# Performance work log

Hardware: AMD Instinct MI355X
Metric: run time of the kernel (lower is better)

Reference implementation:

```python
import jax, jax.numpy as jnp
import numpy as np

E, TOP_K, H, I = 8, 2, 1024, 2048
B, S = 1, 2048


def setup_inputs() -> dict:
    key = jax.random.key(0)
    ks = jax.random.split(key, 5)
    scale_h = 1.0 / np.sqrt(H)
    scale_i = 1.0 / np.sqrt(I)
    return {
        "hidden_states": jax.random.normal(ks[0], (B, S, H), dtype=jnp.float32),
        "gate_w": jax.random.normal(ks[1], (E, H), dtype=jnp.float32) * scale_h,
        "w1": jax.random.normal(ks[2], (E, I, H), dtype=jnp.float32) * scale_h,
        "w3": jax.random.normal(ks[3], (E, I, H), dtype=jnp.float32) * scale_h,
        "w2": jax.random.normal(ks[4], (E, H, I), dtype=jnp.float32) * scale_i,
    }


def _moe(x, gate_w, w1, w3, w2):
    orig_shape = x.shape
    xt = x.reshape(-1, H)                       # [T, H]
    logits = xt @ gate_w.T                      # [T, E] router logits
    probs = jax.nn.softmax(logits, axis=-1)
    topw, topi = jax.lax.top_k(probs, TOP_K)    # [T, K]
    topw = topw / jnp.sum(topw, axis=-1, keepdims=True)  # renormalize=True
    # dense per-token expert weights [T, E]
    ew = jnp.sum(jax.nn.one_hot(topi, E, dtype=xt.dtype) * topw[..., None], axis=1)
    # SwiGLU experts, vectorized over all experts
    g = jnp.einsum('th,eih->tei', xt, w1)       # [T, E, I]
    u = jnp.einsum('th,eih->tei', xt, w3)
    act = jax.nn.silu(g) * u
    ye = jnp.einsum('tei,ehi->teh', act, w2)    # [T, E, H]
    out = jnp.einsum('te,teh->th', ew, ye)      # weighted combine
    return out.reshape(orig_shape)


def reference(hidden_states, gate_w, w1, w3, w2):
    return _moe(hidden_states, gate_w, w1, w3, w2)
```

## Files before the change

kernel.cpp:

```cpp
#include <hip/hip_runtime.h>
#include <hip/hip_bf16.h>
#include <math.h>

#define T_TOK 2048
#define HD 1024
#define ID 2048
#define NE 8

typedef __attribute__((ext_vector_type(8))) short s16x8;
typedef __attribute__((ext_vector_type(8))) unsigned short u16x8;
typedef __attribute__((ext_vector_type(4))) float f32x4;
typedef __attribute__((ext_vector_type(4))) unsigned short u16x4;

__device__ __forceinline__ unsigned short f2bf(float f) {
  union { float f; unsigned u; } v; v.f = f;
  unsigned r = v.u + 0x7FFFu + ((v.u >> 16) & 1u);
  return (unsigned short)(r >> 16);
}

__device__ __forceinline__ s16x8 cvt8(float4 a, float4 b) {
  union { s16x8 v; __hip_bfloat16 h[8]; } u;
  u.h[0] = __float2bfloat16(a.x); u.h[1] = __float2bfloat16(a.y);
  u.h[2] = __float2bfloat16(a.z); u.h[3] = __float2bfloat16(a.w);
  u.h[4] = __float2bfloat16(b.x); u.h[5] = __float2bfloat16(b.y);
  u.h[6] = __float2bfloat16(b.z); u.h[7] = __float2bfloat16(b.w);
  return u.v;
}

#define GLOAD16(gsrc, ldst) \
  __builtin_amdgcn_global_load_lds((const __attribute__((address_space(1))) void*)(gsrc), \
                                   (__attribute__((address_space(3))) void*)(ldst), 16, 0, 0)

#define WAIT_BARRIER() do { \
  asm volatile("s_waitcnt vmcnt(0) lgkmcnt(0)" ::: "memory"); \
  __builtin_amdgcn_s_barrier(); } while (0)

__global__ void router_k(const float* __restrict__ x, const float* __restrict__ gate,
                         int* __restrict__ cnt, int* __restrict__ tok,
                         float* __restrict__ wt, int* __restrict__ inv) {
  int wid = threadIdx.x >> 6, lane = threadIdx.x & 63;
  int t = blockIdx.x * 4 + wid;
  const float* xr = x + (size_t)t * HD;
  float acc[NE];
#pragma unroll
  for (int e = 0; e < NE; e++) acc[e] = 0.f;
  for (int h = lane; h < HD; h += 64) {
    float xv = xr[h];
#pragma unroll
    for (int e = 0; e < NE; e++) acc[e] += xv * gate[e * HD + h];
  }
#pragma unroll
  for (int e = 0; e < NE; e++)
    for (int off = 32; off; off >>= 1) acc[e] += __shfl_xor(acc[e], off);
  int i0 = 0;
#pragma unroll
  for (int e = 1; e < NE; e++) if (acc[e] > acc[i0]) i0 = e;
  int i1 = (i0 == 0) ? 1 : 0;
#pragma unroll
  for (int e = 0; e < NE; e++) if (e != i0 && acc[e] > acc[i1]) i1 = e;
  float w0 = 1.f / (1.f + expf(acc[i1] - acc[i0]));
  float w1 = 1.f - w0;
  if (lane == 0) {
    int p0 = atomicAdd(&cnt[i0], 1);
    tok[i0 * T_TOK + p0] = t; wt[i0 * T_TOK + p0] = w0;
    inv[2 * t] = (i0 << 16) | p0;
    int p1 = atomicAdd(&cnt[i1], 1);
    tok[i1 * T_TOK + p1] = t; wt[i1 * T_TOK + p1] = w1;
    inv[2 * t + 1] = (i1 << 16) | p1;
  }
}

__global__ void prefix_k(const int* __restrict__ cnt, int* __restrict__ offs) {
  if (threadIdx.x == 0) {
    int s = 0;
    for (int e = 0; e < NE; e++) { offs[e] = s; s += cnt[e]; }
  }
}

__global__ void gather_k(const float* __restrict__ x, const int* __restrict__ cnt,
                         const int* __restrict__ offs, const int* __restrict__ tok,
                         unsigned short* __restrict__ Xg) {
  int e = blockIdx.x >> 11, slot = blockIdx.x & 2047;
  if (slot >= cnt[e]) return;
  int t = tok[e * T_TOK + slot];
  int row = offs[e] + slot;
  int c = threadIdx.x * 4;
  float4 f = *(const float4*)(x + (size_t)t * HD + c);
  u16x4 o; o.x = f2bf(f.x); o.y = f2bf(f.y); o.z = f2bf(f.z); o.w = f2bf(f.w);
  *(u16x4*)(Xg + (size_t)row * HD + c) = o;
}

__global__ __launch_bounds__(512, 4) void gemm1_k(
    const unsigned short* __restrict__ Xg, const float* __restrict__ w1,
    const float* __restrict__ w3, const int* __restrict__ cnt,
    const int* __restrict__ offs, const float* __restrict__ wt,
    unsigned short* __restrict__ act) {
  int bid = blockIdx.x;
  int e = bid & 7;
  int r2 = bid >> 3;
  int nt = r2 & 31, mt = r2 >> 5;
  int count = cnt[e];
  if (mt * 256 >= count) return;
  int i0 = nt * 64;
  int rbase = offs[e] + mt * 256;
  const float* W1 = w1 + (size_t)e * ID * HD;
  const float* W3 = w3 + (size_t)e * ID * HD;

  __shared__ __align__(16) unsigned short Ab[2][256 * 32];
  __shared__ __align__(16) float B1b[2][64 * 32];
  __shared__ __align__(16) float B2b[2][64 * 32];

  int tid = threadIdx.x;
  int wid = tid >> 6, lane = tid & 63;
  int wr = wid >> 1, wc = wid & 1;
  int l15 = lane & 15, hi = lane >> 4;

  const unsigned short* aS[2];
#pragma unroll
  for (int c = 0; c < 2; c++)
    aS[c] = Xg + (size_t)(rbase + c * 128 + wid * 16 + (lane >> 2)) * HD
               + (((lane & 3) ^ ((lane >> 2) & 3)) * 8);
  const float* b1S = W1 + (size_t)(i0 + wid * 8 + (lane >> 3)) * HD
                        + (((lane & 7) ^ ((lane >> 3) & 7)) * 4);
  const float* b2S = W3 + (size_t)(i0 + wid * 8 + (lane >> 3)) * HD
                        + (((lane & 7) ^ ((lane >> 3) & 7)) * 4);

  f32x4 accg[4][2], accu[4][2];
#pragma unroll
  for (int m = 0; m < 4; m++)
#pragma unroll
    for (int n = 0; n < 2; n++) {
      accg[m][n] = (f32x4){0.f, 0.f, 0.f, 0.f};
      accu[m][n] = (f32x4){0.f, 0.f, 0.f, 0.f};
    }

  int aswz = (hi ^ (l15 & 3)) * 8;
  int bg0 = ((hi * 2) ^ (l15 & 7)) * 4;
  int bg1 = ((hi * 2 + 1) ^ (l15 & 7)) * 4;

#define G1_STAGE(buf, k0) do { \
    GLOAD16(aS[0] + (k0), &Ab[buf][wid * 512]); \
    GLOAD16(aS[1] + (k0), &Ab[buf][4096 + wid * 512]); \
    GLOAD16(b1S + (k0), &B1b[buf][wid * 256]); \
    GLOAD16(b2S + (k0), &B2b[buf][wid * 256]); } while (0)

  G1_STAGE(0, 0);
  WAIT_BARRIER();

  for (int t = 0; t < 32; ++t) {
    int cur = t & 1;
    if (t < 31) G1_STAGE(cur ^ 1, (t + 1) * 32);
    s16x8 a[4];
#pragma unroll
    for (int m = 0; m < 4; m++)
      a[m] = *(const s16x8*)&Ab[cur][(wr * 64 + m * 16 + l15) * 32 + aswz];
#pragma unroll
    for (int n = 0; n < 2; n++) {
      int rB = (wc * 32 + n * 16 + l15) * 32;
      float4 q0 = *(const float4*)&B1b[cur][rB + bg0];
      float4 q1 = *(const float4*)&B1b[cur][rB + bg1];
      s16x8 b1 = cvt8(q0, q1);
      float4 q2 = *(const float4*)&B2b[cur][rB + bg0];
      float4 q3 = *(const float4*)&B2b[cur][rB + bg1];
      s16x8 b2 = cvt8(q2, q3);
#pragma unroll
      for (int m = 0; m < 4; m++) {
        accg[m][n] = __builtin_amdgcn_mfma_f32_16x16x32_bf16(a[m], b1, accg[m][n], 0, 0, 0);
        accu[m][n] = __builtin_amdgcn_mfma_f32_16x16x32_bf16(a[m], b2, accu[m][n], 0, 0, 0);
      }
    }
    WAIT_BARRIER();
  }

#pragma unroll
  for (int m = 0; m < 4; m++)
#pragma unroll
    for (int r = 0; r < 4; r++) {
      int rl = mt * 256 + wr * 64 + m * 16 + hi * 4 + r;
      if (rl < count) {
        float w = wt[e * T_TOK + rl];
#pragma unroll
        for (int n = 0; n < 2; n++) {
          float g = accg[m][n][r], u = accu[m][n][r];
          float s = (g / (1.f + expf(-g))) * u * w;
          act[(size_t)(offs[e] + rl) * ID + i0 + wc * 32 + n * 16 + l15] =
              (unsigned short)__bfloat16_as_ushort(__float2bfloat16(s));
        }
      }
    }
#undef G1_STAGE
}

__global__ __launch_bounds__(512, 4) void gemm2_k(
    const unsigned short* __restrict__ act, const float* __restrict__ w2,
    const int* __restrict__ cnt, const int* __restrict__ offs,
    float* __restrict__ ye) {
  int bid = blockIdx.x;
  int e = bid & 7;
  int r2 = bid >> 3;
  int nt = r2 & 15, mt = r2 >> 4;
  int count = cnt[e];
  if (mt * 256 >= count) return;
  int h0 = nt * 64;
  int rbase = offs[e] + mt * 256;
  const float* W2 = w2 + (size_t)e * HD * ID;

  __shared__ __align__(16) unsigned short Ab[2][256 * 32];
  __shared__ __align__(16) float Bb[2][64 * 32];

  int tid = threadIdx.x;
  int wid = tid >> 6, lane = tid & 63;
  int wr = wid >> 1, wc = wid & 1;
  int l15 = lane & 15, hi = lane >> 4;

  const unsigned short* aS[2];
#pragma unroll
  for (int c = 0; c < 2; c++)
    aS[c] = act + (size_t)(rbase + c * 128 + wid * 16 + (lane >> 2)) * ID
                + (((lane & 3) ^ ((lane >> 2) & 3)) * 8);
  const float* bS = W2 + (size_t)(h0 + wid * 8 + (lane >> 3)) * ID
                       + (((lane & 7) ^ ((lane >> 3) & 7)) * 4);

  f32x4 acc[4][2];
#pragma unroll
  for (int m = 0; m < 4; m++)
#pragma unroll
    for (int n = 0; n < 2; n++) acc[m][n] = (f32x4){0.f, 0.f, 0.f, 0.f};

  int aswz = (hi ^ (l15 & 3)) * 8;
  int bg0 = ((hi * 2) ^ (l15 & 7)) * 4;
  int bg1 = ((hi * 2 + 1) ^ (l15 & 7)) * 4;

#define G2_STAGE(buf, k0) do { \
    GLOAD16(aS[0] + (k0), &Ab[buf][wid * 512]); \
    GLOAD16(aS[1] + (k0), &Ab[buf][4096 + wid * 512]); \
    GLOAD16(bS + (k0), &Bb[buf][wid * 256]); } while (0)

  G2_STAGE(0, 0);
  WAIT_BARRIER();

  for (int t = 0; t < 64; ++t) {
    int cur = t & 1;
    if (t < 63) G2_STAGE(cur ^ 1, (t + 1) * 32);
    s16x8 a[4];
#pragma unroll
    for (int m = 0; m < 4; m++)
      a[m] = *(const s16x8*)&Ab[cur][(wr * 64 + m * 16 + l15) * 32 + aswz];
#pragma unroll
    for (int n = 0; n < 2; n++) {
      int rB = (wc * 32 + n * 16 + l15) * 32;
      float4 q0 = *(const float4*)&Bb[cur][rB + bg0];
      float4 q1 = *(const float4*)&Bb[cur][rB + bg1];
      s16x8 b = cvt8(q0, q1);
#pragma unroll
      for (int m = 0; m < 4; m++)
        acc[m][n] = __builtin_amdgcn_mfma_f32_16x16x32_bf16(a[m], b, acc[m][n], 0, 0, 0);
    }
    WAIT_BARRIER();
  }

#pragma unroll
  for (int m = 0; m < 4; m++)
#pragma unroll
    for (int r = 0; r < 4; r++) {
      int slot = mt * 256 + wr * 64 + m * 16 + hi * 4 + r;
      if (slot < count) {
#pragma unroll
        for (int n = 0; n < 2; n++)
          ye[(size_t)(offs[e] + slot) * HD + h0 + wc * 32 + n * 16 + l15] = acc[m][n][r];
      }
    }
#undef G2_STAGE
}

__global__ void combine_k(const float* __restrict__ ye, const int* __restrict__ inv,
                          const int* __restrict__ offs, float* __restrict__ out) {
  int t = blockIdx.x;
  int c = threadIdx.x * 4;
  int v0 = inv[2 * t], v1 = inv[2 * t + 1];
  int r0 = offs[v0 >> 16] + (v0 & 0xFFFF);
  int r1 = offs[v1 >> 16] + (v1 & 0xFFFF);
  float4 a = *(const float4*)(ye + (size_t)r0 * HD + c);
  float4 b = *(const float4*)(ye + (size_t)r1 * HD + c);
  float4 o = {a.x + b.x, a.y + b.y, a.z + b.z, a.w + b.w};
  *(float4*)(out + (size_t)t * HD + c) = o;
}

extern "C" void kernel_launch(void* const* d_in, const int* in_sizes, int n_in,
                              void* d_out, int out_size, void* d_ws, size_t ws_size,
                              hipStream_t stream) {
  const float* x    = (const float*)d_in[0];
  const float* gate = (const float*)d_in[1];
  const float* w1   = (const float*)d_in[2];
  const float* w3   = (const float*)d_in[3];
  const float* w2   = (const float*)d_in[4];
  float* out = (float*)d_out;

  char* ws = (char*)d_ws;
  int* cnt  = (int*)(ws + 0);
  int* offs = (int*)(ws + 256);
  int* tok  = (int*)(ws + 512);
  float* wt = (float*)(ws + 66048);
  int* inv  = (int*)(ws + 131584);
  unsigned short* Xg  = (unsigned short*)(ws + 148480);
  unsigned short* act = (unsigned short*)(ws + 10634240);
  float* ye = (float*)(ws + 31605760);

  hipMemsetAsync(cnt, 0, 256, stream);

  router_k<<<T_TOK / 4, 256, 0, stream>>>(x, gate, cnt, tok, wt, inv);
  prefix_k<<<1, 64, 0, stream>>>(cnt, offs);
  gather_k<<<NE * T_TOK, 256, 0, stream>>>(x, cnt, offs, tok, Xg);
  gemm1_k<<<NE * 32 * 4, 512, 0, stream>>>(Xg, w1, w3, cnt, offs, wt, act);
  gemm2_k<<<NE * 16 * 4, 512, 0, stream>>>(act, w2, cnt, offs, ye);
  combine_k<<<T_TOK, 256, 0, stream>>>(ye, inv, offs, out);
}
```

Baseline: 405.4 us.

## Deepen weight prefetch pipeline, relayout LDS tiles, and shrink gemm2 tiles

Both expert GEMMs move from a double-buffered load/compute loop with full vmcnt(0) waits to a deeper pipeline. gemm1 gets a triple-buffered weight stage and gemm2 a quad-buffered one, each waiting with a partial vmcnt and a single barrier per iteration. The LDS layout is changed from XOR-swizzled rows to a k-chunk-major layout that matches the MFMA fragment reads. gemm2 is cut to 256 threads with 128-row tiles and the gemm1 grid is enlarged, which aims to hide global-load latency and raise occupancy at the cost of more LDS, more redundant weight reads, and some fragile wait-count logic.

```diff
diff --git a/kernel.cpp b/kernel.cpp
--- a/kernel.cpp
+++ b/kernel.cpp
@@ -30,10 +30,6 @@
 #define GLOAD16(gsrc, ldst) \
   __builtin_amdgcn_global_load_lds((const __attribute__((address_space(1))) void*)(gsrc), \
                                    (__attribute__((address_space(3))) void*)(ldst), 16, 0, 0)
-
-#define WAIT_BARRIER() do { \
-  asm volatile("s_waitcnt vmcnt(0) lgkmcnt(0)" ::: "memory"); \
-  __builtin_amdgcn_s_barrier(); } while (0)
 
 __global__ void router_k(const float* __restrict__ x, const float* __restrict__ gate,
                          int* __restrict__ cnt, int* __restrict__ tok,
@@ -107,8 +103,8 @@
   const float* W3 = w3 + (size_t)e * ID * HD;
 
   __shared__ __align__(16) unsigned short Ab[2][256 * 32];
-  __shared__ __align__(16) float B1b[2][64 * 32];
-  __shared__ __align__(16) float B2b[2][64 * 32];
+  __shared__ __align__(16) float B1b[3][64 * 32];
+  __shared__ __align__(16) float B2b[3][64 * 32];
 
   int tid = threadIdx.x;
   int wid = tid >> 6, lane = tid & 63;
@@ -118,12 +114,13 @@
   const unsigned short* aS[2];
 #pragma unroll
   for (int c = 0; c < 2; c++)
-    aS[c] = Xg + (size_t)(rbase + c * 128 + wid * 16 + (lane >> 2)) * HD
-               + (((lane & 3) ^ ((lane >> 2) & 3)) * 8);
-  const float* b1S = W1 + (size_t)(i0 + wid * 8 + (lane >> 3)) * HD
-                        + (((lane & 7) ^ ((lane >> 3) & 7)) * 4);
-  const float* b2S = W3 + (size_t)(i0 + wid * 8 + (lane >> 3)) * HD
-                        + (((lane & 7) ^ ((lane >> 3) & 7)) * 4);
+    aS[c] = Xg + (size_t)(rbase + (2 * wid + c) * 16 + l15) * HD + hi * 8;
+  int aD[2];
+#pragma unroll
+  for (int c = 0; c < 2; c++) aD[c] = (2 * wid + c) * 512 + lane * 8;
+  const float* b1S = W1 + (size_t)(i0 + lane) * HD + wid * 4;
+  const float* b2S = W3 + (size_t)(i0 + lane) * HD + wid * 4;
+  int bD = wid * 256 + lane * 4;
 
   f32x4 accg[4][2], accu[4][2];
 #pragma unroll
@@ -134,34 +131,36 @@
       accu[m][n] = (f32x4){0.f, 0.f, 0.f, 0.f};
     }
 
-  int aswz = (hi ^ (l15 & 3)) * 8;
-  int bg0 = ((hi * 2) ^ (l15 & 7)) * 4;
-  int bg1 = ((hi * 2 + 1) ^ (l15 & 7)) * 4;
-
-#define G1_STAGE(buf, k0) do { \
-    GLOAD16(aS[0] + (k0), &Ab[buf][wid * 512]); \
-    GLOAD16(aS[1] + (k0), &Ab[buf][4096 + wid * 512]); \
-    GLOAD16(b1S + (k0), &B1b[buf][wid * 256]); \
-    GLOAD16(b2S + (k0), &B2b[buf][wid * 256]); } while (0)
-
-  G1_STAGE(0, 0);
-  WAIT_BARRIER();
+#define STAGE_A1(buf, k0) do { \
+    GLOAD16(aS[0] + (k0), &Ab[buf][aD[0]]); \
+    GLOAD16(aS[1] + (k0), &Ab[buf][aD[1]]); } while (0)
+#define STAGE_B1(buf, k0) do { \
+    GLOAD16(b1S + (k0), &B1b[buf][bD]); \
+    GLOAD16(b2S + (k0), &B2b[buf][bD]); } while (0)
+
+  STAGE_A1(0, 0);
+  STAGE_B1(0, 0);
+  STAGE_B1(1, 32);
 
   for (int t = 0; t < 32; ++t) {
-    int cur = t & 1;
-    if (t < 31) G1_STAGE(cur ^ 1, (t + 1) * 32);
+    if (t < 31) asm volatile("s_waitcnt vmcnt(2)" ::: "memory");
+    else        asm volatile("s_waitcnt vmcnt(0)" ::: "memory");
+    __builtin_amdgcn_s_barrier();
+    if (t < 31) STAGE_A1((t + 1) & 1, (t + 1) * 32);
+    if (t < 30) STAGE_B1((t + 2) % 3, (t + 2) * 32);
+    int ab = t & 1, bb = t % 3;
     s16x8 a[4];
 #pragma unroll
     for (int m = 0; m < 4; m++)
-      a[m] = *(const s16x8*)&Ab[cur][(wr * 64 + m * 16 + l15) * 32 + aswz];
+      a[m] = *(const s16x8*)&Ab[ab][(wr * 4 + m) * 512 + hi * 128 + l15 * 8];
 #pragma unroll
     for (int n = 0; n < 2; n++) {
-      int rB = (wc * 32 + n * 16 + l15) * 32;
-      float4 q0 = *(const float4*)&B1b[cur][rB + bg0];
-      float4 q1 = *(const float4*)&B1b[cur][rB + bg1];
+      int rB = (wc * 32 + n * 16 + l15) * 4;
+      float4 q0 = *(const float4*)&B1b[bb][(2 * hi) * 256 + rB];
+      float4 q1 = *(const float4*)&B1b[bb][(2 * hi + 1) * 256 + rB];
       s16x8 b1 = cvt8(q0, q1);
-      float4 q2 = *(const float4*)&B2b[cur][rB + bg0];
-      float4 q3 = *(const float4*)&B2b[cur][rB + bg1];
+      float4 q2 = *(const float4*)&B2b[bb][(2 * hi) * 256 + rB];
+      float4 q3 = *(const float4*)&B2b[bb][(2 * hi + 1) * 256 + rB];
       s16x8 b2 = cvt8(q2, q3);
 #pragma unroll
       for (int m = 0; m < 4; m++) {
@@ -169,7 +168,6 @@
         accu[m][n] = __builtin_amdgcn_mfma_f32_16x16x32_bf16(a[m], b2, accu[m][n], 0, 0, 0);
       }
     }
-    WAIT_BARRIER();
   }
 
 #pragma unroll
@@ -183,15 +181,15 @@
         for (int n = 0; n < 2; n++) {
           float g = accg[m][n][r], u = accu[m][n][r];
           float s = (g / (1.f + expf(-g))) * u * w;
-          act[(size_t)(offs[e] + rl) * ID + i0 + wc * 32 + n * 16 + l15] =
-              (unsigned short)__bfloat16_as_ushort(__float2bfloat16(s));
+          act[(size_t)(offs[e] + rl) * ID + i0 + wc * 32 + n * 16 + l15] = f2bf(s);
         }
       }
     }
-#undef G1_STAGE
-}
-
-__global__ __launch_bounds__(512, 4) void gemm2_k(
+#undef STAGE_A1
+#undef STAGE_B1
+}
+
+__global__ __launch_bounds__(256, 3) void gemm2_k(
     const unsigned short* __restrict__ act, const float* __restrict__ w2,
     const int* __restrict__ cnt, const int* __restrict__ offs,
     float* __restrict__ ye) {
@@ -200,13 +198,13 @@
   int r2 = bid >> 3;
   int nt = r2 & 15, mt = r2 >> 4;
   int count = cnt[e];
-  if (mt * 256 >= count) return;
+  if (mt * 128 >= count) return;
   int h0 = nt * 64;
-  int rbase = offs[e] + mt * 256;
+  int rbase = offs[e] + mt * 128;
   const float* W2 = w2 + (size_t)e * HD * ID;
 
-  __shared__ __align__(16) unsigned short Ab[2][256 * 32];
-  __shared__ __align__(16) float Bb[2][64 * 32];
+  __shared__ __align__(16) unsigned short Ab[2][128 * 32];
+  __shared__ __align__(16) float Bb[4][64 * 32];
 
   int tid = threadIdx.x;
   int wid = tid >> 6, lane = tid & 63;
@@ -216,10 +214,17 @@
   const unsigned short* aS[2];
 #pragma unroll
   for (int c = 0; c < 2; c++)
-    aS[c] = act + (size_t)(rbase + c * 128 + wid * 16 + (lane >> 2)) * ID
-                + (((lane & 3) ^ ((lane >> 2) & 3)) * 8);
-  const float* bS = W2 + (size_t)(h0 + wid * 8 + (lane >> 3)) * ID
-                       + (((lane & 7) ^ ((lane >> 3) & 7)) * 4);
+    aS[c] = act + (size_t)(rbase + (2 * wid + c) * 16 + l15) * ID + hi * 8;
+  int aD[2];
+#pragma unroll
+  for (int c = 0; c < 2; c++) aD[c] = (2 * wid + c) * 512 + lane * 8;
+  const float* bS[2];
+#pragma unroll
+  for (int c = 0; c < 2; c++)
+    bS[c] = W2 + (size_t)(h0 + lane) * ID + (2 * wid + c) * 4;
+  int bD[2];
+#pragma unroll
+  for (int c = 0; c < 2; c++) bD[c] = (2 * wid + c) * 256 + lane * 4;
 
   f32x4 acc[4][2];
 #pragma unroll
@@ -227,50 +232,54 @@
 #pragma unroll
     for (int n = 0; n < 2; n++) acc[m][n] = (f32x4){0.f, 0.f, 0.f, 0.f};
 
-  int aswz = (hi ^ (l15 & 3)) * 8;
-  int bg0 = ((hi * 2) ^ (l15 & 7)) * 4;
-  int bg1 = ((hi * 2 + 1) ^ (l15 & 7)) * 4;
-
-#define G2_STAGE(buf, k0) do { \
-    GLOAD16(aS[0] + (k0), &Ab[buf][wid * 512]); \
-    GLOAD16(aS[1] + (k0), &Ab[buf][4096 + wid * 512]); \
-    GLOAD16(bS + (k0), &Bb[buf][wid * 256]); } while (0)
-
-  G2_STAGE(0, 0);
-  WAIT_BARRIER();
+#define STAGE_A2(buf, k0) do { \
+    GLOAD16(aS[0] + (k0), &Ab[buf][aD[0]]); \
+    GLOAD16(aS[1] + (k0), &Ab[buf][aD[1]]); } while (0)
+#define STAGE_B2(buf, k0) do { \
+    GLOAD16(bS[0] + (k0), &Bb[buf][bD[0]]); \
+    GLOAD16(bS[1] + (k0), &Bb[buf][bD[1]]); } while (0)
+
+  STAGE_B2(0, 0);
+  STAGE_B2(1, 32);
+  STAGE_A2(0, 0);
+  STAGE_B2(2, 64);
 
   for (int t = 0; t < 64; ++t) {
-    int cur = t & 1;
-    if (t < 63) G2_STAGE(cur ^ 1, (t + 1) * 32);
+    if (t < 62) asm volatile("s_waitcnt vmcnt(2)" ::: "memory");
+    else        asm volatile("s_waitcnt vmcnt(0)" ::: "memory");
+    __builtin_amdgcn_s_barrier();
+    if (t < 63) STAGE_A2((t + 1) & 1, (t + 1) * 32);
+    if (t < 61) STAGE_B2((t + 3) & 3, (t + 3) * 32);
+    int ab = t & 1, bb = t & 3;
     s16x8 a[4];
 #pragma unroll
     for (int m = 0; m < 4; m++)
-      a[m] = *(const s16x8*)&Ab[cur][(wr * 64 + m * 16 + l15) * 32 + aswz];
+      a[m] = *(const s16x8*)&Ab[ab][(wr * 4 + m) * 512 + hi * 128 + l15 * 8];
 #pragma unroll
     for (int n = 0; n < 2; n++) {
-      int rB = (wc * 32 + n * 16 + l15) * 32;
-      float4 q0 = *(const float4*)&Bb[cur][rB + bg0];
-      float4 q1 = *(const float4*)&Bb[cur][rB + bg1];
+      int rB = (wc * 32 + n * 16 + l15) * 4;
+      float4 q0 = *(const float4*)&Bb[bb][(2 * hi) * 256 + rB];
+      float4 q1 = *(const float4*)&Bb[bb][(2 * hi + 1) * 256 + rB];
       s16x8 b = cvt8(q0, q1);
 #pragma unroll
       for (int m = 0; m < 4; m++)
         acc[m][n] = __builtin_amdgcn_mfma_f32_16x16x32_bf16(a[m], b, acc[m][n], 0, 0, 0);
     }
-    WAIT_BARRIER();
   }
 
 #pragma unroll
   for (int m = 0; m < 4; m++)
 #pragma unroll
     for (int r = 0; r < 4; r++) {
-      int slot = mt * 256 + wr * 64 + m * 16 + hi * 4 + r;
+      int slot = mt * 128 + wr * 64 + m * 16 + hi * 4 + r;
       if (slot < count) {
 #pragma unroll
         for (int n = 0; n < 2; n++)
           ye[(size_t)(offs[e] + slot) * HD + h0 + wc * 32 + n * 16 + l15] = acc[m][n][r];
       }
     }
-#undef G2_STAGE
+#undef STAGE_A2
+#undef STAGE_B2
 }
 
 __global__ void combine_k(const float* __restrict__ ye, const int* __restrict__ inv,
@@ -311,7 +320,7 @@
   router_k<<<T_TOK / 4, 256, 0, stream>>>(x, gate, cnt, tok, wt, inv);
   prefix_k<<<1, 64, 0, stream>>>(cnt, offs);
   gather_k<<<NE * T_TOK, 256, 0, stream>>>(x, cnt, offs, tok, Xg);
-  gemm1_k<<<NE * 32 * 4, 512, 0, stream>>>(Xg, w1, w3, cnt, offs, wt, act);
-  gemm2_k<<<NE * 16 * 4, 512, 0, stream>>>(act, w2, cnt, offs, ye);
+  gemm1_k<<<NE * 32 * 8, 512, 0, stream>>>(Xg, w1, w3, cnt, offs, wt, act);
+  gemm2_k<<<NE * 16 * 16, 256, 0, stream>>>(act, w2, cnt, offs, ye);
   combine_k<<<T_TOK, 256, 0, stream>>>(ye, inv, offs, out);
 }
```

Result: slower. 435.4 us (+7.4%).
